# Optimization experiments

Measured on AMD Instinct MI355X. Metric: run time of the kernel, lower is better.

Reference implementation:

```python
import jax, jax.numpy as jnp
import numpy as np

COMMITMENT_COST = 0.25
NUM_EMBEDDINGS = 512

def _conv(x, w, b=None, stride=1, pad=1):
    y = jax.lax.conv_general_dilated(x, w, (stride, stride), [(pad, pad)] * 2,
                                     dimension_numbers=('NCHW', 'OIHW', 'NCHW'))
    return y if b is None else y + b[None, :, None, None]

def _tconv(x, w, b, stride=2, k=4, p=1):
    # torch ConvTranspose2d(in,out,k,s,p): weight (in,out,kh,kw)
    w2 = jnp.flip(w, (2, 3)).transpose(1, 0, 2, 3)  # -> (out,in,kh,kw)
    pad = k - 1 - p
    y = jax.lax.conv_general_dilated(x, w2, (1, 1), [(pad, pad)] * 2,
                                     lhs_dilation=(stride, stride),
                                     dimension_numbers=('NCHW', 'OIHW', 'NCHW'))
    return y + b[None, :, None, None]

def _residual(x, w1, w2):
    return x + _conv(jax.nn.relu(_conv(jax.nn.relu(x), w1)), w2)

def _res_stack(x, w11, w12, w21, w22):
    x = jax.nn.relu(_residual(x, w11, w12))
    return jax.nn.relu(_residual(x, w21, w22))

def _vq(z, codebook):
    # z: (B, D, H, W) -> NHWC
    inputs = z.transpose(0, 2, 3, 1)
    B, H, W, D = inputs.shape
    flat = inputs.reshape(-1, D)  # (N, D)
    # squared euclidean distances (argmin-equivalent to torch.cdist)
    d2 = (jnp.sum(flat * flat, 1, keepdims=True)
          - 2.0 * flat @ codebook.T
          + jnp.sum(codebook * codebook, 1)[None, :])  # (N, K)
    idx = jnp.argmin(d2, axis=1)
    quantized = codebook[idx].reshape(B, H, W, D)
    sg = jax.lax.stop_gradient
    e_latent_loss = jnp.mean((sg(quantized) - inputs) ** 2)
    q_latent_loss = jnp.mean((quantized - sg(inputs)) ** 2)
    loss = q_latent_loss + COMMITMENT_COST * e_latent_loss
    quantized_st = inputs + sg(quantized - inputs)
    avg_probs = jnp.bincount(idx, length=NUM_EMBEDDINGS).astype(jnp.float32) / flat.shape[0]
    perplexity = jnp.exp(-jnp.sum(avg_probs * jnp.log(avg_probs + 1e-10)))
    return loss, quantized_st.transpose(0, 3, 1, 2), perplexity

def setup_inputs() -> dict:
    key = jax.random.key(0)
    ks = jax.random.split(key, 24)
    Hc, D, K = 128, 64, NUM_EMBEDDINGS
    s = 0.05
    rn = lambda k, sh: (jax.random.normal(k, sh, jnp.float32) * s)
    inp = {
        'x': jax.random.normal(ks[0], (32, 3, 256, 256), jnp.float32),
        # encoder
        'e1w': rn(ks[1], (Hc // 2, 3, 4, 4)), 'e1b': rn(ks[2], (Hc // 2,)),
        'e2w': rn(ks[3], (Hc, Hc // 2, 4, 4)), 'e2b': rn(ks[4], (Hc,)),
        'er11': rn(ks[5], (Hc, Hc, 3, 3)), 'er12': rn(ks[6], (Hc, Hc, 3, 3)),
        'er21': rn(ks[7], (Hc, Hc, 3, 3)), 'er22': rn(ks[8], (Hc, Hc, 3, 3)),
        # pre-vq conv 1x1
        'pvw': rn(ks[9], (D, Hc, 1, 1)), 'pvb': rn(ks[10], (D,)),
        # codebook: uniform(-1/K, 1/K)
        'cb': jax.random.uniform(ks[11], (K, D), jnp.float32, -1.0 / K, 1.0 / K),
        # decoder
        'd1w': rn(ks[12], (Hc, D, 3, 3)), 'd1b': rn(ks[13], (Hc,)),
        'dr11': rn(ks[14], (Hc, Hc, 3, 3)), 'dr12': rn(ks[15], (Hc, Hc, 3, 3)),
        'dr21': rn(ks[16], (Hc, Hc, 3, 3)), 'dr22': rn(ks[17], (Hc, Hc, 3, 3)),
        't1w': rn(ks[18], (Hc, Hc // 2, 4, 4)), 't1b': rn(ks[19], (Hc // 2,)),
        't2w': rn(ks[20], (Hc // 2, 3, 4, 4)), 't2b': rn(ks[21], (3,)),
    }
    return inp

def reference(x, e1w, e1b, e2w, e2b, er11, er12, er21, er22, pvw, pvb, cb,
              d1w, d1b, dr11, dr12, dr21, dr22, t1w, t1b, t2w, t2b):
    # encoder
    z = jax.nn.relu(_conv(x, e1w, e1b, stride=2, pad=1))
    z = _conv(z, e2w, e2b, stride=2, pad=1)
    z = _res_stack(z, er11, er12, er21, er22)
    # pre-vq 1x1 conv
    z = _conv(z, pvw, pvb, stride=1, pad=0)
    # vector quantization
    loss, quantized, perplexity = _vq(z, cb)
    # decoder
    h = _conv(quantized, d1w, d1b, stride=1, pad=1)
    h = _res_stack(h, dr11, dr12, dr21, dr22)
    h = jax.nn.relu(_tconv(h, t1w, t1b))
    x_recon = _tconv(h, t2w, t2b)
    return loss, x_recon, perplexity
```

## Files before the change

kernel.cpp:

```cpp
#include <hip/hip_runtime.h>

typedef short bf16x8 __attribute__((ext_vector_type(8)));
typedef float f32x4 __attribute__((ext_vector_type(4)));
typedef unsigned short ushort4v __attribute__((ext_vector_type(4)));
typedef unsigned int u32x4 __attribute__((ext_vector_type(4)));

__device__ __forceinline__ unsigned short f2bf(float f) {
  unsigned u = __float_as_uint(f);
  unsigned r = (u + 0x7FFFu + ((u >> 16) & 1u)) >> 16;
  return (unsigned short)r;
}
__device__ __forceinline__ float bf2f(unsigned short u) {
  return __uint_as_float(((unsigned)u) << 16);
}

__device__ __forceinline__ bf16x8 relu_bf8(bf16x8 v) {
  u32x4 u;
  __builtin_memcpy(&u, &v, 16);
  #pragma unroll
  for (int i = 0; i < 4; i++) {
    unsigned s = u[i] & 0x80008000u;
    u[i] &= ~((s >> 15) * 0xFFFFu);
  }
  bf16x8 r;
  __builtin_memcpy(&r, &u, 16);
  return r;
}

__device__ __forceinline__ int xcd_swz(int bid, int n) {
  return (bid & 7) * (n >> 3) + (bid >> 3);
}

__global__ void init_k(int* __restrict__ hist) {
  int t = threadIdx.x;
  if (t < 512) hist[t] = 0;
}

__global__ void cbh_k(const float* __restrict__ cb, float* __restrict__ cbh) {
  int k = blockIdx.x * 256 + threadIdx.x;
  if (k >= 512) return;
  const float* c = cb + k * 64;
  float s = 0.f;
  #pragma unroll
  for (int d = 0; d < 64; d++) s = fmaf(c[d], c[d], s);
  cbh[k] = 0.5f * s;
}

__global__ void repack_cbf_k(const float* __restrict__ cb,
                             unsigned short* __restrict__ cbf) {
  int idx = blockIdx.x * 256 + threadIdx.x;
  if (idx >= 32768) return;
  int j = idx & 7;
  int lane = (idx >> 3) & 63;
  int ks = (idx >> 9) & 1;
  int m = idx >> 10;
  int code = m * 16 + (lane & 15);
  int d = ks * 32 + (lane >> 4) * 8 + j;
  cbf[idx] = f2bf(cb[code * 64 + d]);
}

template <int CIN>
__global__ void repack_frag_k(const float* __restrict__ w,
                              unsigned short* __restrict__ wf) {
  int idx = blockIdx.x * 256 + threadIdx.x;
  int total = (CIN / 32) * 9 * 8 * 512;
  if (idx >= total) return;
  int j = idx & 7;
  int lane = (idx >> 3) & 63;
  int M = (idx >> 9) & 7;
  int tk = idx >> 12;
  int tap = tk % 9;
  int kstep = tk / 9;
  int co = M * 16 + (lane & 15);
  int ci = kstep * 32 + (lane >> 4) * 8 + j;
  wf[idx] = f2bf(w[((size_t)co * CIN + ci) * 9 + tap]);
}

__global__ void repack_e1f_k(const float* __restrict__ w,
                             unsigned short* __restrict__ wf) {
  int idx = blockIdx.x * 256 + threadIdx.x;
  if (idx >= 4096) return;
  int j = idx & 7;
  int lane = (idx >> 3) & 63;
  int m = (idx >> 9) & 3;
  int ks = idx >> 11;
  int co = m * 16 + (lane & 15);
  int k = ks * 32 + (lane >> 4) * 8 + j;
  float v = (k < 48) ? w[co * 48 + k] : 0.f;
  wf[idx] = f2bf(v);
}

__global__ void repack_e2f_k(const float* __restrict__ w,
                             unsigned short* __restrict__ wf) {
  int idx = blockIdx.x * 256 + threadIdx.x;
  if (idx >= 131072) return;
  int j = idx & 7;
  int lane = (idx >> 3) & 63;
  int M = (idx >> 9) & 7;
  int tap = (idx >> 12) & 15;
  int ks = idx >> 16;
  int co = M * 16 + (lane & 15);
  int ci = ks * 32 + (lane >> 4) * 8 + j;
  wf[idx] = f2bf(w[((size_t)co * 64 + ci) * 16 + tap]);
}

__global__ void repack_pvf_k(const float* __restrict__ w,
                             unsigned short* __restrict__ wf) {
  int idx = blockIdx.x * 256 + threadIdx.x;
  if (idx >= 8192) return;
  int j = idx & 7;
  int lane = (idx >> 3) & 63;
  int m = (idx >> 9) & 3;
  int ks = idx >> 11;
  int co = m * 16 + (lane & 15);
  int ci = ks * 32 + (lane >> 4) * 8 + j;
  wf[idx] = f2bf(w[co * 128 + ci]);
}

__global__ void repack_t1f_k(const float* __restrict__ w,
                             unsigned short* __restrict__ wf) {
  int idx = blockIdx.x * 256 + threadIdx.x;
  if (idx >= 131072) return;
  int j = idx & 7;
  int lane = (idx >> 3) & 63;
  int m = (idx >> 9) & 3;
  int tap = (idx >> 11) & 3;
  int ks = (idx >> 13) & 3;
  int par = (idx >> 15) & 3;
  int sy = par >> 1, sx = par & 1;
  int ty = tap >> 1, tx = tap & 1;
  int ky = sy ? (ty ? 0 : 2) : (ty ? 1 : 3);
  int kx = sx ? (tx ? 0 : 2) : (tx ? 1 : 3);
  int co = m * 16 + (lane & 15);
  int ci = ks * 32 + (lane >> 4) * 8 + j;
  wf[idx] = f2bf(w[((size_t)ci * 64 + co) * 16 + ky * 4 + kx]);
}

__global__ void repack_t2f_k(const float* __restrict__ w,
                             unsigned short* __restrict__ wf) {
  int idx = blockIdx.x * 256 + threadIdx.x;
  if (idx >= 16384) return;
  int j = idx & 7;
  int lane = (idx >> 3) & 63;
  int tap = (idx >> 9) & 3;
  int ks = (idx >> 11) & 1;
  int par = idx >> 12;
  int sy = par >> 1, sx = par & 1;
  int ty = tap >> 1, tx = tap & 1;
  int ky = sy ? (ty ? 0 : 2) : (ty ? 1 : 3);
  int kx = sx ? (tx ? 0 : 2) : (tx ? 1 : 3);
  int co = lane & 15;
  int ci = ks * 32 + (lane >> 4) * 8 + j;
  float v = (co < 3) ? w[((size_t)ci * 3 + co) * 16 + ky * 4 + kx] : 0.f;
  wf[idx] = f2bf(v);
}

__global__ __launch_bounds__(256, 4) void e1m_k(
    const float* __restrict__ x, const unsigned short* __restrict__ wf,
    const float* __restrict__ bias, unsigned short* __restrict__ out) {
  __shared__ unsigned short patch[128 * 72];
  int blk = xcd_swz(blockIdx.x, gridDim.x);
  int b = blk >> 7;
  int oy = blk & 127;
  int t = threadIdx.x;
  int w = t >> 6, l = t & 63;
  int cib = (l >> 4) * 8, colb = l & 15;
  const float* xb = x + (size_t)b * 3 * 65536;
  {
    int p = t & 127;
    int kb = (t >> 7) * 32;
    int px2 = 2 * p - 1;
    int oy2 = 2 * oy - 1;
    bf16x8 pk[4];
    #pragma unroll
    for (int c = 0; c < 4; c++) {
      #pragma unroll
      for (int j = 0; j < 8; j++) {
        int k = kb + c * 8 + j;
        float v = 0.f;
        if (k < 48) {
          int ci = k >> 4;
          int ky = (k >> 2) & 3, kx = k & 3;
          int iy = oy2 + ky, ix = px2 + kx;
          if ((unsigned)iy < 256u && (unsigned)ix < 256u)
            v = xb[ci * 65536 + iy * 256 + ix];
        }
        pk[c][j] = (short)f2bf(v);
      }
    }
    unsigned short* row = &patch[p * 72 + kb];
    #pragma unroll
    for (int c = 0; c < 4; c++)
      *(bf16x8*)&row[c * 8] = pk[c];
  }
  __syncthreads();
  f32x4 acc[8];
  #pragma unroll
  for (int n = 0; n < 8; n++) acc[n] = (f32x4){0.f, 0.f, 0.f, 0.f};
  #pragma unroll
  for (int ks = 0; ks < 2; ks++) {
    bf16x8 af = *(const bf16x8*)&wf[((size_t)(ks * 4 + w) * 64 + l) * 8];
    #pragma unroll
    for (int n = 0; n < 8; n++) {
      bf16x8 bfrag =
          *(const bf16x8*)&patch[(n * 16 + colb) * 72 + ks * 32 + cib];
      acc[n] = __builtin_amdgcn_mfma_f32_16x16x32_bf16(af, bfrag, acc[n],
                                                       0, 0, 0);
    }
  }
  int cob = w * 16 + (l >> 4) * 4;
  f32x4 bj = *(const f32x4*)&bias[cob];
  #pragma unroll
  for (int n = 0; n < 8; n++) {
    int p = n * 16 + colb;
    ushort4v pk = {f2bf(fmaxf(acc[n][0] + bj[0], 0.f)),
                   f2bf(fmaxf(acc[n][1] + bj[1], 0.f)),
                   f2bf(fmaxf(acc[n][2] + bj[2], 0.f)),
                   f2bf(fmaxf(acc[n][3] + bj[3], 0.f))};
    *(ushort4v*)&out[((size_t)b * 16384 + oy * 128 + p) * 64 + cob] = pk;
  }
}

__global__ __launch_bounds__(256, 4) void e2m_k(
    const unsigned short* __restrict__ in,
    const unsigned short* __restrict__ wf, const float* __restrict__ bias,
    unsigned short* __restrict__ out) {
  __shared__ unsigned short patch[528 * 36];
  int blk = xcd_swz(blockIdx.x, gridDim.x);
  int b = blk >> 6;
  int oy = blk & 63;
  int t = threadIdx.x;
  int w = t >> 6, l = t & 63;
  int cib = (l >> 4) * 8, colb = l & 15;
  f32x4 acc[2][4];
  #pragma unroll
  for (int m = 0; m < 2; m++)
    #pragma unroll
    for (int n = 0; n < 4; n++) acc[m][n] = (f32x4){0.f, 0.f, 0.f, 0.f};
  const unsigned short* inb = in + (size_t)b * 16384 * 64;
  for (int ks = 0; ks < 2; ks++) {
    __syncthreads();
    for (int idx = t; idx < 2112; idx += 256) {
      int q = idx & 3;
      int pos = idx >> 2;
      int r = pos / 132, c = pos - r * 132;
      int iy = 2 * oy - 1 + r, ix = c - 1;
      bf16x8 v = (bf16x8){0, 0, 0, 0, 0, 0, 0, 0};
      if ((unsigned)iy < 128u && (unsigned)ix < 128u)
        v = *(const bf16x8*)&inb[((size_t)iy * 128 + ix) * 64 + ks * 32 + q * 8];
      int s = (c >> 1) + (c & 1) * 66;
      *(bf16x8*)&patch[(r * 132 + s) * 36 + q * 8] = v;
    }
    __syncthreads();
    __builtin_amdgcn_s_setprio(1);
    #pragma unroll
    for (int tap = 0; tap < 16; tap++) {
      int ky = tap >> 2, kx = tap & 3;
      bf16x8 bfrag[4];
      #pragma unroll
      for (int n = 0; n < 4; n++) {
        int ox = n * 16 + colb;
        int pos = ky * 132 + (kx & 1) * 66 + ox + (kx >> 1);
        bfrag[n] = *(const bf16x8*)&patch[pos * 36 + cib];
      }
      const unsigned short* wft = wf + ((size_t)(ks * 16 + tap) * 8) * 512;
      #pragma unroll
      for (int m = 0; m < 2; m++) {
        bf16x8 af = *(const bf16x8*)&wft[((w * 2 + m) * 64 + l) * 8];
        #pragma unroll
        for (int n = 0; n < 4; n++)
          acc[m][n] = __builtin_amdgcn_mfma_f32_16x16x32_bf16(af, bfrag[n],
                                                              acc[m][n], 0, 0, 0);
      }
    }
    __builtin_amdgcn_s_setprio(0);
  }
  #pragma unroll
  for (int m = 0; m < 2; m++) {
    int cob = (w * 2 + m) * 16 + (l >> 4) * 4;
    f32x4 bj = *(const f32x4*)&bias[cob];
    #pragma unroll
    for (int n = 0; n < 4; n++) {
      int ox = n * 16 + colb;
      size_t adr = ((size_t)(b * 4096 + oy * 64 + ox)) * 128 + cob;
      ushort4v pre = {f2bf(acc[m][n][0] + bj[0]), f2bf(acc[m][n][1] + bj[1]),
                      f2bf(acc[m][n][2] + bj[2]), f2bf(acc[m][n][3] + bj[3])};
      *(ushort4v*)&out[adr] = pre;
    }
  }
}

template <int CIN, bool RES_ADD, bool RELU_IN, bool HAS_BIAS, bool PRE_ONLY>
__global__ __launch_bounds__(256, 4) void conv3nh_k(
    const unsigned short* __restrict__ in,
    const unsigned short* __restrict__ wf,
    const float* __restrict__ bias,
    const unsigned short* __restrict__ res,
    unsigned short* __restrict__ out) {
  constexpr int KSTEPS = CIN / 32;
  __shared__ unsigned short patch[264 * 40];
  int blk = xcd_swz(blockIdx.x, gridDim.x);
  int b = blk >> 5;
  int tile = blk & 31;
  int y0 = tile * 2;
  int t = threadIdx.x;
  int w = t >> 6, l = t & 63;
  int wm = w >> 1, wn = w & 1;
  int n0 = wn * 64;
  int cib = (l >> 4) * 8, colb = l & 15;
  f32x4 acc[4][4];
  #pragma unroll
  for (int m = 0; m < 4; m++)
    #pragma unroll
    for (int n = 0; n < 4; n++) acc[m][n] = (f32x4){0.f, 0.f, 0.f, 0.f};
  const unsigned short* inb = in + (size_t)b * 4096 * CIN;
  for (int ks = 0; ks < KSTEPS; ks++) {
    __syncthreads();
    for (int idx = t; idx < 1056; idx += 256) {
      int q = idx & 3;
      int pos = idx >> 2;
      int r = pos / 66, c = pos - r * 66;
      int y = y0 - 1 + r, x = c - 1;
      bf16x8 v = (bf16x8){0, 0, 0, 0, 0, 0, 0, 0};
      if ((unsigned)y < 64u && (unsigned)x < 64u)
        v = *(const bf16x8*)&inb[((size_t)(y * 64 + x)) * CIN + ks * 32 + q * 8];
      if (RELU_IN) v = relu_bf8(v);
      *(bf16x8*)&patch[pos * 40 + q * 8] = v;
    }
    __syncthreads();
    __builtin_amdgcn_s_setprio(1);
    const unsigned short* wfk = wf + (size_t)ks * 9 * 4096;
    #pragma unroll
    for (int tap = 0; tap < 9; tap++) {
      int ky = tap / 3, kx = tap % 3;
      bf16x8 bfrag[4];
      #pragma unroll
      for (int n = 0; n < 4; n++) {
        int p = n0 + n * 16 + colb;
        int pr = p >> 6, pc = p & 63;
        int pos = (pr + ky) * 66 + (pc + kx);
        bfrag[n] = *(const bf16x8*)&patch[pos * 40 + cib];
      }
      const unsigned short* wft = wfk + tap * 4096;
      bf16x8 afrag[4];
      #pragma unroll
      for (int m = 0; m < 4; m++)
        afrag[m] = *(const bf16x8*)&wft[((wm * 4 + m) * 64 + l) * 8];
      #pragma unroll
      for (int m = 0; m < 4; m++)
        #pragma unroll
        for (int n = 0; n < 4; n++)
          acc[m][n] = __builtin_amdgcn_mfma_f32_16x16x32_bf16(
              afrag[m], bfrag[n], acc[m][n], 0, 0, 0);
    }
    __builtin_amdgcn_s_setprio(0);
  }
  #pragma unroll
  for (int m = 0; m < 4; m++) {
    int cobase = wm * 64 + m * 16 + (l >> 4) * 4;
    float b0 = HAS_BIAS ? bias[cobase] : 0.f;
    float b1 = HAS_BIAS ? bias[cobase + 1] : 0.f;
    float b2 = HAS_BIAS ? bias[cobase + 2] : 0.f;
    float b3 = HAS_BIAS ? bias[cobase + 3] : 0.f;
    #pragma unroll
    for (int n = 0; n < 4; n++) {
      int p = n0 + n * 16 + colb;
      size_t adr = ((size_t)(b * 4096 + tile * 128 + p)) * 128 + cobase;
      float f0 = acc[m][n][0] + b0, f1 = acc[m][n][1] + b1;
      float f2 = acc[m][n][2] + b2, f3 = acc[m][n][3] + b3;
      if (RES_ADD) {
        ushort4v rv = *(const ushort4v*)&res[adr];
        f0 += bf2f(rv.x); f1 += bf2f(rv.y); f2 += bf2f(rv.z); f3 += bf2f(rv.w);
      }
      ushort4v pk;
      if (PRE_ONLY) {
        pk.x = f2bf(f0); pk.y = f2bf(f1); pk.z = f2bf(f2); pk.w = f2bf(f3);
      } else {
        pk.x = f2bf(fmaxf(f0, 0.f)); pk.y = f2bf(fmaxf(f1, 0.f));
        pk.z = f2bf(fmaxf(f2, 0.f)); pk.w = f2bf(fmaxf(f3, 0.f));
      }
      *(ushort4v*)&out[adr] = pk;
    }
  }
}

__global__ __launch_bounds__(256, 4) void pvqm_k(
    const unsigned short* __restrict__ in,
    const unsigned short* __restrict__ wf, const float* __restrict__ bias,
    unsigned short* __restrict__ z) {
  int blk = blockIdx.x;
  int b = blk >> 4;
  int hw0 = (blk & 15) * 256;
  int t = threadIdx.x;
  int w = t >> 6, l = t & 63;
  int n0 = w * 64;
  int cib = (l >> 4) * 8, colb = l & 15;
  f32x4 acc[4][4];
  #pragma unroll
  for (int m = 0; m < 4; m++)
    #pragma unroll
    for (int n = 0; n < 4; n++) acc[m][n] = (f32x4){0.f, 0.f, 0.f, 0.f};
  const unsigned short* inb = in + ((size_t)(b * 4096 + hw0)) * 128;
  for (int ks = 0; ks < 4; ks++) {
    bf16x8 bfrag[4];
    #pragma unroll
    for (int n = 0; n < 4; n++) {
      int p = n0 + n * 16 + colb;
      bfrag[n] = *(const bf16x8*)&inb[(size_t)p * 128 + ks * 32 + cib];
    }
    const unsigned short* wk = wf + ks * 4 * 512;
    #pragma unroll
    for (int m = 0; m < 4; m++) {
      bf16x8 af = *(const bf16x8*)&wk[(m * 64 + l) * 8];
      #pragma unroll
      for (int n = 0; n < 4; n++)
        acc[m][n] = __builtin_amdgcn_mfma_f32_16x16x32_bf16(af, bfrag[n],
                                                            acc[m][n], 0, 0, 0);
    }
  }
  #pragma unroll
  for (int m = 0; m < 4; m++) {
    int cob = m * 16 + (l >> 4) * 4;
    f32x4 bj = *(const f32x4*)&bias[cob];
    #pragma unroll
    for (int n = 0; n < 4; n++) {
      int p = n0 + n * 16 + colb;
      ushort4v pk = {f2bf(acc[m][n][0] + bj[0]), f2bf(acc[m][n][1] + bj[1]),
                     f2bf(acc[m][n][2] + bj[2]), f2bf(acc[m][n][3] + bj[3])};
      *(ushort4v*)&z[((size_t)(b * 4096 + hw0 + p)) * 64 + cob] = pk;
    }
  }
}

__global__ __launch_bounds__(256, 2) void vq_argmin_k(
    const unsigned short* __restrict__ z,
    const unsigned short* __restrict__ cbf, const float* __restrict__ cbh,
    unsigned short* __restrict__ bidx) {
  __shared__ unsigned short bidx_s[256];
  int blk = blockIdx.x;
  int b = blk >> 4;
  int hw0 = (blk & 15) * 256;
  int t = threadIdx.x;
  int w = t >> 6, l = t & 63;
  int colb = l & 15, cib = (l >> 4) * 8;
  const unsigned short* zb = z + ((size_t)(b * 4096 + hw0)) * 64;
  bf16x8 bfrag[4][2];
  #pragma unroll
  for (int n = 0; n < 4; n++) {
    int p = w * 64 + n * 16 + colb;
    #pragma unroll
    for (int ks = 0; ks < 2; ks++)
      bfrag[n][ks] = *(const bf16x8*)&zb[(size_t)p * 64 + ks * 32 + cib];
  }
  float best[4];
  int bid[4];
  #pragma unroll
  for (int n = 0; n < 4; n++) { best[n] = -1e30f; bid[n] = 0; }
  for (int m = 0; m < 32; m++) {
    bf16x8 a0 = *(const bf16x8*)&cbf[((size_t)(m * 2 + 0) * 64 + l) * 8];
    bf16x8 a1 = *(const bf16x8*)&cbf[((size_t)(m * 2 + 1) * 64 + l) * 8];
    int code0 = m * 16 + (l >> 4) * 4;
    f32x4 ch = *(const f32x4*)&cbh[code0];
    #pragma unroll
    for (int n = 0; n < 4; n++) {
      f32x4 acc = (f32x4){0.f, 0.f, 0.f, 0.f};
      acc = __builtin_amdgcn_mfma_f32_16x16x32_bf16(a0, bfrag[n][0], acc, 0, 0, 0);
      acc = __builtin_amdgcn_mfma_f32_16x16x32_bf16(a1, bfrag[n][1], acc, 0, 0, 0);
      #pragma unroll
      for (int r = 0; r < 4; r++) {
        float sc = acc[r] - ch[r];
        if (sc > best[n]) { best[n] = sc; bid[n] = code0 + r; }
      }
    }
  }
  #pragma unroll
  for (int n = 0; n < 4; n++) {
    #pragma unroll
    for (int off = 16; off <= 32; off <<= 1) {
      float ob = __shfl_xor(best[n], off, 64);
      int oi = __shfl_xor(bid[n], off, 64);
      if (ob > best[n] || (ob == best[n] && oi < bid[n])) {
        best[n] = ob;
        bid[n] = oi;
      }
    }
    if ((l >> 4) == 0) bidx_s[w * 64 + n * 16 + colb] = (unsigned short)bid[n];
  }
  __syncthreads();
  bidx[(size_t)b * 4096 + hw0 + t] = bidx_s[t];
}

__global__ __launch_bounds__(256, 4) void vq_apply_k(
    const unsigned short* __restrict__ z,
    const float* __restrict__ cb, const unsigned short* __restrict__ bidx,
    unsigned short* __restrict__ q,
    float* __restrict__ part, int part_off) {
  __shared__ float red[256];
  int blk = blockIdx.x;
  int t = threadIdx.x;
  size_t pxg = (size_t)blk * 256 + t;
  int bi = bidx[pxg];
  const float* cq = cb + bi * 64;
  const unsigned short* zp = z + pxg * 64;
  unsigned short* qp = q + pxg * 64;
  float ls = 0.f;
  #pragma unroll
  for (int g = 0; g < 8; g++) {
    u32x4 zv = *(const u32x4*)&zp[g * 8];
    u32x4 qv;
    #pragma unroll
    for (int h = 0; h < 4; h++) {
      int d = g * 8 + h * 2;
      float q0 = cq[d], q1 = cq[d + 1];
      float z0 = __uint_as_float(zv[h] << 16);
      float z1 = __uint_as_float(zv[h] & 0xFFFF0000u);
      float d0 = q0 - z0, d1 = q1 - z1;
      ls = fmaf(d0, d0, ls);
      ls = fmaf(d1, d1, ls);
      qv[h] = (unsigned)f2bf(q0) | ((unsigned)f2bf(q1) << 16);
    }
    *(u32x4*)&qp[g * 8] = qv;
  }
  red[t] = ls;
  __syncthreads();
  for (int s = 128; s > 0; s >>= 1) {
    if (t < s) red[t] += red[t + s];
    __syncthreads();
  }
  if (t == 0) part[part_off + blk] = red[0];
}

__global__ __launch_bounds__(1024) void vq_hist_k(
    const unsigned short* __restrict__ bidx, int* __restrict__ hist) {
  __shared__ int hl[512];
  int t = threadIdx.x;
  if (t < 512) hl[t] = 0;
  __syncthreads();
  int base = blockIdx.x * 16384;
  for (int i = t; i < 16384; i += 1024)
    atomicAdd(&hl[bidx[base + i]], 1);
  __syncthreads();
  if (t < 512 && hl[t] > 0) atomicAdd(&hist[t], hl[t]);
}

__global__ __launch_bounds__(256, 2) void t1m_k(
    const unsigned short* __restrict__ in,
    const unsigned short* __restrict__ wf, const float* __restrict__ bias,
    unsigned short* __restrict__ out) {
  __shared__ unsigned short patch[264 * 36];
  int blk = xcd_swz(blockIdx.x, gridDim.x);
  int b = blk >> 5;
  int a0 = (blk & 31) * 2;
  int t = threadIdx.x;
  int w = t >> 6, l = t & 63;
  int sy = w >> 1, sx = w & 1;
  int cib = (l >> 4) * 8, colb = l & 15;
  f32x4 acc[4][8];
  #pragma unroll
  for (int m = 0; m < 4; m++)
    #pragma unroll
    for (int n = 0; n < 8; n++) acc[m][n] = (f32x4){0.f, 0.f, 0.f, 0.f};
  const unsigned short* inb = in + (size_t)b * 4096 * 128;
  for (int ks = 0; ks < 4; ks++) {
    __syncthreads();
    for (int idx = t; idx < 1056; idx += 256) {
      int q = idx & 3;
      int pos = idx >> 2;
      int r = pos / 66, c = pos - r * 66;
      int y = a0 - 1 + r, x = c - 1;
      bf16x8 v = (bf16x8){0, 0, 0, 0, 0, 0, 0, 0};
      if ((unsigned)y < 64u && (unsigned)x < 64u)
        v = *(const bf16x8*)&inb[((size_t)(y * 64 + x)) * 128 + ks * 32 + q * 8];
      *(bf16x8*)&patch[pos * 36 + q * 8] = v;
    }
    __syncthreads();
    __builtin_amdgcn_s_setprio(1);
    const unsigned short* wpar = wf + (size_t)((sy * 2 + sx) * 4 + ks) * 8192;
    #pragma unroll
    for (int tap = 0; tap < 4; tap++) {
      int ty = tap >> 1, tx = tap & 1;
      int d = sy ? ty + 1 : ty;
      int e = sx ? tx + 1 : tx;
      bf16x8 bfrag[8];
      #pragma unroll
      for (int n = 0; n < 8; n++) {
        int p = n * 16 + colb;
        int ar = p >> 6, pc = p & 63;
        int pos = (ar + d) * 66 + (pc + e);
        bfrag[n] = *(const bf16x8*)&patch[pos * 36 + cib];
      }
      bf16x8 afrag[4];
      #pragma unroll
      for (int m = 0; m < 4; m++)
        afrag[m] = *(const bf16x8*)&wpar[(tap * 256 + m * 64 + l) * 8];
      #pragma unroll
      for (int m = 0; m < 4; m++)
        #pragma unroll
        for (int n = 0; n < 8; n++)
          acc[m][n] = __builtin_amdgcn_mfma_f32_16x16x32_bf16(
              afrag[m], bfrag[n], acc[m][n], 0, 0, 0);
    }
    __builtin_amdgcn_s_setprio(0);
  }
  #pragma unroll
  for (int m = 0; m < 4; m++) {
    int cob = m * 16 + (l >> 4) * 4;
    float b0 = bias[cob], b1 = bias[cob + 1], b2 = bias[cob + 2],
          b3 = bias[cob + 3];
    #pragma unroll
    for (int n = 0; n < 8; n++) {
      int p = n * 16 + colb;
      int ar = p >> 6, pc = p & 63;
      int oy = 2 * (a0 + ar) + sy, ox = 2 * pc + sx;
      ushort4v pk;
      pk.x = f2bf(fmaxf(acc[m][n][0] + b0, 0.f));
      pk.y = f2bf(fmaxf(acc[m][n][1] + b1, 0.f));
      pk.z = f2bf(fmaxf(acc[m][n][2] + b2, 0.f));
      pk.w = f2bf(fmaxf(acc[m][n][3] + b3, 0.f));
      *(ushort4v*)&out[((size_t)b * 16384 + oy * 128 + ox) * 64 + cob] = pk;
    }
  }
}

__global__ __launch_bounds__(256, 2) void t2m_k(
    const unsigned short* __restrict__ in,
    const unsigned short* __restrict__ wf,
    const float* __restrict__ bias, float* __restrict__ out) {
  __shared__ unsigned short patch[528 * 36];
  int blk = xcd_swz(blockIdx.x, gridDim.x);
  int b = blk >> 6;
  int a0 = (blk & 63) * 2;
  int t = threadIdx.x;
  int w = t >> 6, l = t & 63;
  int sy = w >> 1, sx = w & 1;
  int cib = (l >> 4) * 8, colb = l & 15;
  f32x4 acc[2][8];
  #pragma unroll
  for (int ar = 0; ar < 2; ar++)
    #pragma unroll
    for (int n = 0; n < 8; n++) acc[ar][n] = (f32x4){0.f, 0.f, 0.f, 0.f};
  bf16x8 af[2][4];
  #pragma unroll
  for (int ks = 0; ks < 2; ks++) {
    const unsigned short* wpar = wf + (size_t)((sy * 2 + sx) * 2 + ks) * 2048;
    #pragma unroll
    for (int tap = 0; tap < 4; tap++)
      af[ks][tap] = *(const bf16x8*)&wpar[(tap * 64 + l) * 8];
  }
  const unsigned short* inb = in + (size_t)b * 16384 * 64;
  for (int ks = 0; ks < 2; ks++) {
    __syncthreads();
    for (int idx = t; idx < 2112; idx += 256) {
      int q = idx & 3;
      int pos = idx >> 2;
      int r = pos / 132, c = pos - r * 132;
      int y = a0 - 1 + r, x = c - 1;
      bf16x8 v = (bf16x8){0, 0, 0, 0, 0, 0, 0, 0};
      if ((unsigned)y < 128u && (unsigned)x < 128u)
        v = *(const bf16x8*)&inb[((size_t)(y * 128 + x)) * 64 + ks * 32 + q * 8];
      *(bf16x8*)&patch[pos * 36 + q * 8] = v;
    }
    __syncthreads();
    __builtin_amdgcn_s_setprio(1);
    #pragma unroll
    for (int tap = 0; tap < 4; tap++) {
      int ty = tap >> 1, tx = tap & 1;
      int d = sy ? ty + 1 : ty;
      int e = sx ? tx + 1 : tx;
      #pragma unroll
      for (int ar = 0; ar < 2; ar++) {
        #pragma unroll
        for (int n = 0; n < 8; n++) {
          int pc = n * 16 + colb;
          int pos = (ar + d) * 132 + (pc + e);
          bf16x8 bfrag = *(const bf16x8*)&patch[pos * 36 + cib];
          acc[ar][n] = __builtin_amdgcn_mfma_f32_16x16x32_bf16(
              af[ks][tap], bfrag, acc[ar][n], 0, 0, 0);
        }
      }
    }
    __builtin_amdgcn_s_setprio(0);
  }
  int rb = (l >> 4) * 4;
  #pragma unroll
  for (int r = 0; r < 4; r++) {
    int co = rb + r;
    if (co < 3) {
      float bj = bias[co];
      #pragma unroll
      for (int ar = 0; ar < 2; ar++) {
        int oy = 2 * (a0 + ar) + sy;
        #pragma unroll
        for (int n = 0; n < 8; n++) {
          int pc = n * 16 + colb;
          int ox = 2 * pc + sx;
          out[((size_t)(b * 3 + co)) * 65536 + oy * 256 + ox] = acc[ar][n][r] + bj;
        }
      }
    }
  }
}

__global__ __launch_bounds__(512) void fin_k(
    const float* __restrict__ part, const int* __restrict__ hist,
    float* __restrict__ loss_out, float* __restrict__ perp_out) {
  __shared__ float red[512];
  int t = threadIdx.x;
  red[t] = part[t];
  __syncthreads();
  for (int s = 256; s > 0; s >>= 1) {
    if (t < s) red[t] += red[t + s];
    __syncthreads();
  }
  float loss = 1.25f * red[0] / 8388608.f;
  __syncthreads();
  float p = (float)hist[t] / 131072.f;
  red[t] = -p * logf(p + 1e-10f);
  __syncthreads();
  for (int s = 256; s > 0; s >>= 1) {
    if (t < s) red[t] += red[t + s];
    __syncthreads();
  }
  if (t == 0) {
    *loss_out = loss;
    *perp_out = expf(red[0]);
  }
}

extern "C" void kernel_launch(void* const* d_in, const int* in_sizes, int n_in,
                              void* d_out, int out_size, void* d_ws, size_t ws_size,
                              hipStream_t stream) {
  (void)in_sizes; (void)n_in; (void)out_size;
  const float* x    = (const float*)d_in[0];
  const float* e1w  = (const float*)d_in[1];
  const float* e1b  = (const float*)d_in[2];
  const float* e2w  = (const float*)d_in[3];
  const float* e2b  = (const float*)d_in[4];
  const float* er11 = (const float*)d_in[5];
  const float* er12 = (const float*)d_in[6];
  const float* er21 = (const float*)d_in[7];
  const float* er22 = (const float*)d_in[8];
  const float* pvw  = (const float*)d_in[9];
  const float* pvb  = (const float*)d_in[10];
  const float* cb   = (const float*)d_in[11];
  const float* d1w  = (const float*)d_in[12];
  const float* d1b  = (const float*)d_in[13];
  const float* dr11 = (const float*)d_in[14];
  const float* dr12 = (const float*)d_in[15];
  const float* dr21 = (const float*)d_in[16];
  const float* dr22 = (const float*)d_in[17];
  const float* t1w  = (const float*)d_in[18];
  const float* t1b  = (const float*)d_in[19];
  const float* t2w  = (const float*)d_in[20];
  const float* t2b  = (const float*)d_in[21];
  float* out = (float*)d_out;

  const size_t W_PVF  = 0;
  const size_t W_E2F  = W_PVF + 4096;
  const size_t W_T1F  = W_E2F + 65536;
  const size_t W_T2F  = W_T1F + 65536;
  const size_t W_D1F  = W_T2F + 8192;
  const size_t W_CBF  = W_D1F + 36864;
  const size_t W_E1F  = W_CBF + 16384;
  const size_t W_RT   = W_E1F + 2048;
  const size_t W_CBH  = W_RT + 8 * 73728;
  const size_t W_PART = W_CBH + 512;
  const size_t W_BIDX = W_PART + 512;
  const size_t W_HIST = W_BIDX + 65536;
  const size_t W_TOT  = W_HIST + 512;

  float* ws = (float*)d_ws;
  unsigned short* pvf = (unsigned short*)(ws + W_PVF);
  unsigned short* e2f = (unsigned short*)(ws + W_E2F);
  unsigned short* t1f = (unsigned short*)(ws + W_T1F);
  unsigned short* t2f = (unsigned short*)(ws + W_T2F);
  unsigned short* d1f = (unsigned short*)(ws + W_D1F);
  unsigned short* cbf = (unsigned short*)(ws + W_CBF);
  unsigned short* e1f = (unsigned short*)(ws + W_E1F);
  unsigned short* rtf[8];
  for (int i = 0; i < 8; i++)
    rtf[i] = (unsigned short*)(ws + W_RT + (size_t)i * 73728);
  float* cbh  = ws + W_CBH;
  float* part = ws + W_PART;
  unsigned short* bidx = (unsigned short*)(ws + W_BIDX);
  int*   hist = (int*)(ws + W_HIST);

  size_t wfloats = ws_size / sizeof(float);
  int BC = 32;
  while (BC > 1 && W_TOT + (size_t)BC * 1572864 > wfloats) BC >>= 1;
  int nchunk = 32 / BC;

  unsigned short* E1  = (unsigned short*)(ws + W_TOT);
  unsigned short* P1  = (unsigned short*)(ws + W_TOT + (size_t)BC * 524288);
  unsigned short* P2  = P1 + (size_t)BC * 524288;
  unsigned short* P4  = P2 + (size_t)BC * 524288;
  unsigned short* Zbf = P4 + (size_t)BC * 524288;
  unsigned short* Qbf = Zbf + (size_t)BC * 262144;

  init_k<<<1, 512, 0, stream>>>(hist);
  cbh_k<<<2, 256, 0, stream>>>(cb, cbh);
  repack_cbf_k<<<128, 256, 0, stream>>>(cb, cbf);

  repack_e1f_k<<<16, 256, 0, stream>>>(e1w, e1f);
  repack_pvf_k<<<32, 256, 0, stream>>>(pvw, pvf);
  repack_e2f_k<<<512, 256, 0, stream>>>(e2w, e2f);
  repack_t1f_k<<<512, 256, 0, stream>>>(t1w, t1f);
  repack_t2f_k<<<64, 256, 0, stream>>>(t2w, t2f);
  repack_frag_k<64><<<288, 256, 0, stream>>>(d1w, d1f);
  repack_frag_k<128><<<576, 256, 0, stream>>>(er11, rtf[0]);
  repack_frag_k<128><<<576, 256, 0, stream>>>(er12, rtf[1]);
  repack_frag_k<128><<<576, 256, 0, stream>>>(er21, rtf[2]);
  repack_frag_k<128><<<576, 256, 0, stream>>>(er22, rtf[3]);
  repack_frag_k<128><<<576, 256, 0, stream>>>(dr11, rtf[4]);
  repack_frag_k<128><<<576, 256, 0, stream>>>(dr12, rtf[5]);
  repack_frag_k<128><<<576, 256, 0, stream>>>(dr21, rtf[6]);
  repack_frag_k<128><<<576, 256, 0, stream>>>(dr22, rtf[7]);

  for (int c = 0; c < nchunk; ++c) {
    const float* xc = x + (size_t)c * BC * 3 * 65536;
    float* outc = out + 1 + (size_t)c * BC * 3 * 65536;
    unsigned short* bidxc = bidx + (size_t)c * BC * 4096;
    e1m_k<<<BC * 128, 256, 0, stream>>>(xc, e1f, e1b, E1);
    e2m_k<<<BC * 64, 256, 0, stream>>>(E1, e2f, e2b, P1);
    conv3nh_k<128, false, true,  false, false><<<BC * 32, 256, 0, stream>>>(P1, rtf[0], nullptr, nullptr, P4);
    conv3nh_k<128, true,  false, false, false><<<BC * 32, 256, 0, stream>>>(P4, rtf[1], nullptr, P1, P2);
    conv3nh_k<128, false, false, false, false><<<BC * 32, 256, 0, stream>>>(P2, rtf[2], nullptr, nullptr, P4);
    conv3nh_k<128, true,  false, false, false><<<BC * 32, 256, 0, stream>>>(P4, rtf[3], nullptr, P2, P1);
    pvqm_k<<<BC * 16, 256, 0, stream>>>(P1, pvf, pvb, Zbf);
    vq_argmin_k<<<BC * 16, 256, 0, stream>>>(Zbf, cbf, cbh, bidxc);
    vq_apply_k<<<BC * 16, 256, 0, stream>>>(Zbf, cb, bidxc, Qbf, part, c * BC * 16);
    conv3nh_k<64,  false, false, true,  true ><<<BC * 32, 256, 0, stream>>>(Qbf, d1f, d1b, nullptr, P1);
    conv3nh_k<128, false, true,  false, false><<<BC * 32, 256, 0, stream>>>(P1, rtf[4], nullptr, nullptr, P4);
    conv3nh_k<128, true,  false, false, false><<<BC * 32, 256, 0, stream>>>(P4, rtf[5], nullptr, P1, P2);
    conv3nh_k<128, false, false, false, false><<<BC * 32, 256, 0, stream>>>(P2, rtf[6], nullptr, nullptr, P4);
    conv3nh_k<128, true,  false, false, false><<<BC * 32, 256, 0, stream>>>(P4, rtf[7], nullptr, P2, P1);
    t1m_k<<<BC * 32, 256, 0, stream>>>(P1, t1f, t1b, E1);
    t2m_k<<<BC * 64, 256, 0, stream>>>(E1, t2f, t2b, outc);
  }
  vq_hist_k<<<8, 1024, 0, stream>>>(bidx, hist);
  fin_k<<<1, 512, 0, stream>>>(part, hist, out, out + 1 + 6291456);
}
```

Baseline: 649.0 us.

## Fuse pre-VQ 1x1 conv, VQ argmin and VQ apply into one kernel

Merges the pre-VQ projection, the codebook argmin and the quantize/loss kernels into a single kernel. The z tile is staged in padded shared memory instead of being written to and re-read from global memory, which also removes two launches per chunk. In exchange the fused kernel uses more LDS and a lower occupancy bound, and these three stages are a small part of the total pipeline.

```diff
diff --git a/kernel.cpp b/kernel.cpp
--- a/kernel.cpp
+++ b/kernel.cpp
@@ -384,10 +384,17 @@
   }
 }
 
-__global__ __launch_bounds__(256, 4) void pvqm_k(
+__global__ __launch_bounds__(256, 2) void vqf_k(
     const unsigned short* __restrict__ in,
     const unsigned short* __restrict__ wf, const float* __restrict__ bias,
-    unsigned short* __restrict__ z) {
+    const unsigned short* __restrict__ cbf, const float* __restrict__ cbh,
+    const float* __restrict__ cb,
+    unsigned short* __restrict__ q,
+    unsigned short* __restrict__ bidx,
+    float* __restrict__ part, int part_off) {
+  __shared__ unsigned short zt[256 * 72];
+  __shared__ unsigned short bidx_s[256];
+  __shared__ float red[256];
   int blk = blockIdx.x;
   int b = blk >> 4;
   int hw0 = (blk & 15) * 256;
@@ -395,139 +402,121 @@
   int w = t >> 6, l = t & 63;
   int n0 = w * 64;
   int cib = (l >> 4) * 8, colb = l & 15;
-  f32x4 acc[4][4];
-  #pragma unroll
-  for (int m = 0; m < 4; m++)
-    #pragma unroll
-    for (int n = 0; n < 4; n++) acc[m][n] = (f32x4){0.f, 0.f, 0.f, 0.f};
-  const unsigned short* inb = in + ((size_t)(b * 4096 + hw0)) * 128;
-  for (int ks = 0; ks < 4; ks++) {
-    bf16x8 bfrag[4];
+  {
+    f32x4 acc[4][4];
+    #pragma unroll
+    for (int m = 0; m < 4; m++)
+      #pragma unroll
+      for (int n = 0; n < 4; n++) acc[m][n] = (f32x4){0.f, 0.f, 0.f, 0.f};
+    const unsigned short* inb = in + ((size_t)(b * 4096 + hw0)) * 128;
+    for (int ks = 0; ks < 4; ks++) {
+      bf16x8 bfrag[4];
+      #pragma unroll
+      for (int n = 0; n < 4; n++) {
+        int p = n0 + n * 16 + colb;
+        bfrag[n] = *(const bf16x8*)&inb[(size_t)p * 128 + ks * 32 + cib];
+      }
+      const unsigned short* wk = wf + ks * 4 * 512;
+      #pragma unroll
+      for (int m = 0; m < 4; m++) {
+        bf16x8 af = *(const bf16x8*)&wk[(m * 64 + l) * 8];
+        #pragma unroll
+        for (int n = 0; n < 4; n++)
+          acc[m][n] = __builtin_amdgcn_mfma_f32_16x16x32_bf16(af, bfrag[n],
+                                                              acc[m][n], 0, 0, 0);
+      }
+    }
+    #pragma unroll
+    for (int m = 0; m < 4; m++) {
+      int d0 = m * 16 + (l >> 4) * 4;
+      f32x4 bj = *(const f32x4*)&bias[d0];
+      #pragma unroll
+      for (int n = 0; n < 4; n++) {
+        int p = n0 + n * 16 + colb;
+        ushort4v pk = {f2bf(acc[m][n][0] + bj[0]), f2bf(acc[m][n][1] + bj[1]),
+                       f2bf(acc[m][n][2] + bj[2]), f2bf(acc[m][n][3] + bj[3])};
+        *(ushort4v*)&zt[p * 72 + d0] = pk;
+      }
+    }
+  }
+  __syncthreads();
+  {
+    bf16x8 zfrag[4][2];
     #pragma unroll
     for (int n = 0; n < 4; n++) {
       int p = n0 + n * 16 + colb;
-      bfrag[n] = *(const bf16x8*)&inb[(size_t)p * 128 + ks * 32 + cib];
-    }
-    const unsigned short* wk = wf + ks * 4 * 512;
-    #pragma unroll
-    for (int m = 0; m < 4; m++) {
-      bf16x8 af = *(const bf16x8*)&wk[(m * 64 + l) * 8];
-      #pragma unroll
-      for (int n = 0; n < 4; n++)
-        acc[m][n] = __builtin_amdgcn_mfma_f32_16x16x32_bf16(af, bfrag[n],
-                                                            acc[m][n], 0, 0, 0);
-    }
-  }
-  #pragma unroll
-  for (int m = 0; m < 4; m++) {
-    int cob = m * 16 + (l >> 4) * 4;
-    f32x4 bj = *(const f32x4*)&bias[cob];
+      #pragma unroll
+      for (int k2 = 0; k2 < 2; k2++)
+        zfrag[n][k2] = *(const bf16x8*)&zt[p * 72 + k2 * 32 + cib];
+    }
+    float best[4];
+    int bid[4];
+    #pragma unroll
+    for (int n = 0; n < 4; n++) { best[n] = -1e30f; bid[n] = 0; }
+    for (int m = 0; m < 32; m++) {
+      bf16x8 a0 = *(const bf16x8*)&cbf[((size_t)(m * 2 + 0) * 64 + l) * 8];
+      bf16x8 a1 = *(const bf16x8*)&cbf[((size_t)(m * 2 + 1) * 64 + l) * 8];
+      int code0 = m * 16 + (l >> 4) * 4;
+      f32x4 ch = *(const f32x4*)&cbh[code0];
+      #pragma unroll
+      for (int n = 0; n < 4; n++) {
+        f32x4 acc2 = (f32x4){0.f, 0.f, 0.f, 0.f};
+        acc2 = __builtin_amdgcn_mfma_f32_16x16x32_bf16(a0, zfrag[n][0], acc2, 0, 0, 0);
+        acc2 = __builtin_amdgcn_mfma_f32_16x16x32_bf16(a1, zfrag[n][1], acc2, 0, 0, 0);
+        #pragma unroll
+        for (int r = 0; r < 4; r++) {
+          float sc = acc2[r] - ch[r];
+          if (sc > best[n]) { best[n] = sc; bid[n] = code0 + r; }
+        }
+      }
+    }
     #pragma unroll
     for (int n = 0; n < 4; n++) {
-      int p = n0 + n * 16 + colb;
-      ushort4v pk = {f2bf(acc[m][n][0] + bj[0]), f2bf(acc[m][n][1] + bj[1]),
-                     f2bf(acc[m][n][2] + bj[2]), f2bf(acc[m][n][3] + bj[3])};
-      *(ushort4v*)&z[((size_t)(b * 4096 + hw0 + p)) * 64 + cob] = pk;
-    }
-  }
-}
-
-__global__ __launch_bounds__(256, 2) void vq_argmin_k(
-    const unsigned short* __restrict__ z,
-    const unsigned short* __restrict__ cbf, const float* __restrict__ cbh,
-    unsigned short* __restrict__ bidx) {
-  __shared__ unsigned short bidx_s[256];
-  int blk = blockIdx.x;
-  int b = blk >> 4;
-  int hw0 = (blk & 15) * 256;
-  int t = threadIdx.x;
-  int w = t >> 6, l = t & 63;
-  int colb = l & 15, cib = (l >> 4) * 8;
-  const unsigned short* zb = z + ((size_t)(b * 4096 + hw0)) * 64;
-  bf16x8 bfrag[4][2];
-  #pragma unroll
-  for (int n = 0; n < 4; n++) {
-    int p = w * 64 + n * 16 + colb;
-    #pragma unroll
-    for (int ks = 0; ks < 2; ks++)
-      bfrag[n][ks] = *(const bf16x8*)&zb[(size_t)p * 64 + ks * 32 + cib];
-  }
-  float best[4];
-  int bid[4];
-  #pragma unroll
-  for (int n = 0; n < 4; n++) { best[n] = -1e30f; bid[n] = 0; }
-  for (int m = 0; m < 32; m++) {
-    bf16x8 a0 = *(const bf16x8*)&cbf[((size_t)(m * 2 + 0) * 64 + l) * 8];
-    bf16x8 a1 = *(const bf16x8*)&cbf[((size_t)(m * 2 + 1) * 64 + l) * 8];
-    int code0 = m * 16 + (l >> 4) * 4;
-    f32x4 ch = *(const f32x4*)&cbh[code0];
-    #pragma unroll
-    for (int n = 0; n < 4; n++) {
-      f32x4 acc = (f32x4){0.f, 0.f, 0.f, 0.f};
-      acc = __builtin_amdgcn_mfma_f32_16x16x32_bf16(a0, bfrag[n][0], acc, 0, 0, 0);
-      acc = __builtin_amdgcn_mfma_f32_16x16x32_bf16(a1, bfrag[n][1], acc, 0, 0, 0);
-      #pragma unroll
-      for (int r = 0; r < 4; r++) {
-        float sc = acc[r] - ch[r];
-        if (sc > best[n]) { best[n] = sc; bid[n] = code0 + r; }
-      }
-    }
-  }
-  #pragma unroll
-  for (int n = 0; n < 4; n++) {
-    #pragma unroll
-    for (int off = 16; off <= 32; off <<= 1) {
-      float ob = __shfl_xor(best[n], off, 64);
-      int oi = __shfl_xor(bid[n], off, 64);
-      if (ob > best[n] || (ob == best[n] && oi < bid[n])) {
-        best[n] = ob;
-        bid[n] = oi;
-      }
-    }
-    if ((l >> 4) == 0) bidx_s[w * 64 + n * 16 + colb] = (unsigned short)bid[n];
+      #pragma unroll
+      for (int off = 16; off <= 32; off <<= 1) {
+        float ob = __shfl_xor(best[n], off, 64);
+        int oi = __shfl_xor(bid[n], off, 64);
+        if (ob > best[n] || (ob == best[n] && oi < bid[n])) {
+          best[n] = ob;
+          bid[n] = oi;
+        }
+      }
+      if ((l >> 4) == 0) bidx_s[n0 + n * 16 + colb] = (unsigned short)bid[n];
+    }
   }
   __syncthreads();
-  bidx[(size_t)b * 4096 + hw0 + t] = bidx_s[t];
-}
-
-__global__ __launch_bounds__(256, 4) void vq_apply_k(
-    const unsigned short* __restrict__ z,
-    const float* __restrict__ cb, const unsigned short* __restrict__ bidx,
-    unsigned short* __restrict__ q,
-    float* __restrict__ part, int part_off) {
-  __shared__ float red[256];
-  int blk = blockIdx.x;
-  int t = threadIdx.x;
-  size_t pxg = (size_t)blk * 256 + t;
-  int bi = bidx[pxg];
-  const float* cq = cb + bi * 64;
-  const unsigned short* zp = z + pxg * 64;
-  unsigned short* qp = q + pxg * 64;
-  float ls = 0.f;
-  #pragma unroll
-  for (int g = 0; g < 8; g++) {
-    u32x4 zv = *(const u32x4*)&zp[g * 8];
-    u32x4 qv;
-    #pragma unroll
-    for (int h = 0; h < 4; h++) {
-      int d = g * 8 + h * 2;
-      float q0 = cq[d], q1 = cq[d + 1];
-      float z0 = __uint_as_float(zv[h] << 16);
-      float z1 = __uint_as_float(zv[h] & 0xFFFF0000u);
-      float d0 = q0 - z0, d1 = q1 - z1;
-      ls = fmaf(d0, d0, ls);
-      ls = fmaf(d1, d1, ls);
-      qv[h] = (unsigned)f2bf(q0) | ((unsigned)f2bf(q1) << 16);
-    }
-    *(u32x4*)&qp[g * 8] = qv;
-  }
-  red[t] = ls;
-  __syncthreads();
-  for (int s = 128; s > 0; s >>= 1) {
-    if (t < s) red[t] += red[t + s];
-    __syncthreads();
-  }
-  if (t == 0) part[part_off + blk] = red[0];
+  int bi = bidx_s[t];
+  bidx[(size_t)b * 4096 + hw0 + t] = (unsigned short)bi;
+  {
+    const float* cq = cb + bi * 64;
+    unsigned short* qp = q + ((size_t)(b * 4096 + hw0 + t)) * 64;
+    const unsigned short* zp = &zt[t * 72];
+    float ls = 0.f;
+    #pragma unroll
+    for (int g = 0; g < 8; g++) {
+      u32x4 zv = *(const u32x4*)&zp[g * 8];
+      u32x4 qv;
+      #pragma unroll
+      for (int h = 0; h < 4; h++) {
+        int d = g * 8 + h * 2;
+        float q0 = cq[d], q1 = cq[d + 1];
+        float z0 = __uint_as_float(zv[h] << 16);
+        float z1 = __uint_as_float(zv[h] & 0xFFFF0000u);
+        float d0 = q0 - z0, d1 = q1 - z1;
+        ls = fmaf(d0, d0, ls);
+        ls = fmaf(d1, d1, ls);
+        qv[h] = (unsigned)f2bf(q0) | ((unsigned)f2bf(q1) << 16);
+      }
+      *(u32x4*)&qp[g * 8] = qv;
+    }
+    red[t] = ls;
+    __syncthreads();
+    for (int s = 128; s > 0; s >>= 1) {
+      if (t < s) red[t] += red[t + s];
+      __syncthreads();
+    }
+    if (t == 0) part[part_off + blk] = red[0];
+  }
 }
 
 __global__ __launch_bounds__(1024) void vq_hist_k(
@@ -826,9 +815,8 @@
     conv3nh_k<128, true,  false, false, false><<<BC * 32, 256, 0, stream>>>(P4, rtf[1], nullptr, P1, P2);
     conv3nh_k<128, false, false, false, false><<<BC * 32, 256, 0, stream>>>(P2, rtf[2], nullptr, nullptr, P4);
     conv3nh_k<128, true,  false, false, false><<<BC * 32, 256, 0, stream>>>(P4, rtf[3], nullptr, P2, P1);
-    pvqm_k<<<BC * 16, 256, 0, stream>>>(P1, pvf, pvb, Zbf);
-    vq_argmin_k<<<BC * 16, 256, 0, stream>>>(Zbf, cbf, cbh, bidxc);
-    vq_apply_k<<<BC * 16, 256, 0, stream>>>(Zbf, cb, bidxc, Qbf, part, c * BC * 16);
+    vqf_k<<<BC * 16, 256, 0, stream>>>(P1, pvf, pvb, cbf, cbh, cb, Qbf, bidxc,
+                                       part, c * BC * 16);
     conv3nh_k<64,  false, false, true,  true ><<<BC * 32, 256, 0, stream>>>(Qbf, d1f, d1b, nullptr, P1);
     conv3nh_k<128, false, true,  false, false><<<BC * 32, 256, 0, stream>>>(P1, rtf[4], nullptr, nullptr, P4);
     conv3nh_k<128, true,  false, false, false><<<BC * 32, 256, 0, stream>>>(P4, rtf[5], nullptr, P1, P2);
```

Result: faster. 624.5 us (-3.8%).
